# Kernel optimization log

Hardware: AMD Instinct MI355X
Metric: run time of the kernel (lower is better)

The kernel has to match this reference:

```python
import jax, jax.numpy as jnp
import numpy as np

N = 32768      # total nodes (2048 graphs * 16 nodes)
E = 491520     # total edges (2048 graphs * 16*15)
F = 11         # in_node_nf
H = 64         # hidden_nf
G = 2048       # number of graphs
NN = 16        # nodes per graph
R = 1024       # n_reactions
L = 4          # n_layers
EIN = 2 * H + 1        # edge_mlp input: [h[row], h[col], radial]
NIN = H + H + F        # node_mlp input: [h, agg, node_attr=h0]


def setup_inputs() -> dict:
    key = jax.random.key(0)
    ks = jax.random.split(key, 24)
    s = 0.05
    d = {
        "h0": jax.random.normal(ks[0], (N, F), jnp.float32),
        "positions": jax.random.normal(ks[1], (N, 3), jnp.float32),
        "edges": jax.random.randint(ks[2], (2, E), 0, N),
        "node_mask": jnp.ones((N, 1), jnp.float32),
        "edge_mask": jnp.ones((E, 1), jnp.float32),
        "reaction_indexes": jax.random.randint(ks[3], (G,), 0, R),
        "reaction_signs": jax.random.normal(ks[4], (G,), jnp.float32),
        # params
        "emb_w": jax.random.normal(ks[5], (F, H), jnp.float32) * s,
        "emb_b": jnp.zeros((H,), jnp.float32),
        "edge_w1": jax.random.normal(ks[6], (L, EIN, H), jnp.float32) * s,
        "edge_b1": jnp.zeros((L, H), jnp.float32),
        "edge_w2": jax.random.normal(ks[7], (L, H, H), jnp.float32) * s,
        "edge_b2": jnp.zeros((L, H), jnp.float32),
        "node_w1": jax.random.normal(ks[8], (L, NIN, H), jnp.float32) * s,
        "node_b1": jnp.zeros((L, H), jnp.float32),
        "node_w2": jax.random.normal(ks[9], (L, H, H), jnp.float32) * s,
        "node_b2": jnp.zeros((L, H), jnp.float32),
        "dec_w1": jax.random.normal(ks[10], (H, H), jnp.float32) * s,
        "dec_b1": jnp.zeros((H,), jnp.float32),
        "dec_w2": jax.random.normal(ks[11], (H, H), jnp.float32) * s,
        "dec_b2": jnp.zeros((H,), jnp.float32),
        "g_w1": jax.random.normal(ks[12], (H, H), jnp.float32) * s,
        "g_b1": jnp.zeros((H,), jnp.float32),
        "g_w2": jax.random.normal(ks[13], (H, 1), jnp.float32) * s,
        "g_b2": jnp.zeros((1,), jnp.float32),
        "n_nodes": NN,
        "n_reactions": R,
    }
    return d


def reference(h0, positions, edges, node_mask, edge_mask, reaction_indexes,
              reaction_signs, emb_w, emb_b, edge_w1, edge_b1, edge_w2, edge_b2,
              node_w1, node_b1, node_w2, node_b2, dec_w1, dec_b1, dec_w2,
              dec_b2, g_w1, g_b1, g_w2, g_b2, n_nodes, n_reactions):
    silu = jax.nn.silu
    row, col = edges[0], edges[1]
    n = h0.shape[0]

    # radial is constant across layers (coords never updated in this variant)
    coord_diff = positions[row] - positions[col]          # [E, 3]
    radial = jnp.sum(coord_diff ** 2, axis=1, keepdims=True)  # [E, 1]

    h = h0 @ emb_w + emb_b                                # [N, H]
    for i in range(edge_w1.shape[0]):
        # edge model
        e_in = jnp.concatenate([h[row], h[col], radial], axis=1)  # [E, 2H+1]
        e = silu(e_in @ edge_w1[i] + edge_b1[i])
        e = silu(e @ edge_w2[i] + edge_b2[i])             # [E, H]
        e = e * edge_mask
        # scatter-sum aggregation by source node
        agg = jax.ops.segment_sum(e, row, num_segments=n)  # [N, H]
        # node model (node_attr = h0)
        n_in = jnp.concatenate([h, agg, h0], axis=1)      # [N, 2H+F]
        h = silu(n_in @ node_w1[i] + node_b1[i]) @ node_w2[i] + node_b2[i]

    # node decoder
    h = silu(h @ dec_w1 + dec_b1) @ dec_w2 + dec_b2
    h = h * node_mask
    # pool per graph (fixed n_nodes per graph)
    hg = h.reshape(-1, n_nodes, h.shape[-1]).sum(axis=1)  # [G, H]
    # graph decoder
    temp = silu(hg @ g_w1 + g_b1) @ g_w2 + g_b2           # [G, 1]
    # signed per-reaction aggregation
    pred = jnp.zeros((n_reactions,), h.dtype).at[reaction_indexes].add(
        temp[:, 0] * reaction_signs)
    return pred
```

## Files before the change

kernel.cpp:

```cpp
#include <hip/hip_runtime.h>
#include <math.h>

#define N_NODES 32768
#define N_EDGES 491520
#define F_IN    11
#define H       64
#define G_GRAPHS 2048
#define NN_PER_G 16
#define R_REACT 1024
#define L_LAYERS 4
#define EIN     129
#define NIN     139
#define NPBLK   32

typedef __attribute__((ext_vector_type(8))) short short8;
typedef __attribute__((ext_vector_type(4))) float f32x4;

__device__ __forceinline__ float silu_f(float x) {
    return x * __builtin_amdgcn_rcpf(1.0f + __expf(-x));
}
__device__ __forceinline__ void atomAddF(float* p, float v) {
    unsafeAtomicAdd(p, v);
}
__device__ __forceinline__ float bf2f(unsigned short b) {
    union { float f; unsigned u; } v; v.u = ((unsigned)b) << 16;
    return v.f;
}
__device__ __forceinline__ unsigned short f2bf(float x) {
    union { float f; unsigned u; } v; v.f = x;
    unsigned r = v.u + 0x7FFFu + ((v.u >> 16) & 1u);
    return (unsigned short)(r >> 16);
}
__device__ __forceinline__ void splitbf(float x, unsigned short& hi, unsigned short& lo) {
    hi = f2bf(x);
    lo = f2bf(x - bf2f(hi));
}
__device__ __forceinline__ void splitbf_t(float x, unsigned short& hi, unsigned short& lo) {
    union { float f; unsigned u; } v; v.f = x;
    hi = (unsigned short)(v.u >> 16);
    union { float f; unsigned u; } w; w.f = x - bf2f(hi);
    lo = (unsigned short)(w.u >> 16);
}

__global__ __launch_bounds__(256) void k_embed(
        const float* __restrict__ h0, const float* __restrict__ emb_w,
        const float* __restrict__ emb_b, float* __restrict__ h) {
    int tid = blockIdx.x * 256 + threadIdx.x;
    int n = tid >> 6, j = tid & 63;
    float acc = emb_b[j];
#pragma unroll
    for (int k = 0; k < F_IN; ++k)
        acc += h0[n * F_IN + k] * emb_w[k * H + j];
    h[tid] = acc;
}

__global__ __launch_bounds__(256) void k_radial(
        const int* __restrict__ edges, const float* __restrict__ pos,
        float* __restrict__ radial) {
    int e = blockIdx.x * 256 + threadIdx.x;
    int r = edges[e], c = edges[N_EDGES + e];
    float dx = pos[r * 3 + 0] - pos[c * 3 + 0];
    float dy = pos[r * 3 + 1] - pos[c * 3 + 1];
    float dz = pos[r * 3 + 2] - pos[c * 3 + 2];
    radial[e] = dx * dx + dy * dy + dz * dz;
}

__global__ __launch_bounds__(256) void k_hist(
        const int* __restrict__ edges, int* __restrict__ deg) {
    int e = blockIdx.x * 256 + threadIdx.x;
    atomicAdd(&deg[edges[e]], 1);
}

__global__ __launch_bounds__(128) void k_scan_blk(
        const int* __restrict__ deg, int* __restrict__ off,
        int* __restrict__ bsum) {
    __shared__ int sd[128];
    int b = blockIdx.x;
    sd[threadIdx.x] = deg[b * 128 + threadIdx.x];
    __syncthreads();
    if (threadIdx.x == 0) {
        int s = 0;
        for (int i = 0; i < 128; ++i) { int d = sd[i]; sd[i] = s; s += d; }
        bsum[b] = s;
    }
    __syncthreads();
    off[b * 128 + threadIdx.x] = sd[threadIdx.x];
}

__global__ __launch_bounds__(256) void k_scan_top(
        const int* __restrict__ bsum, int* __restrict__ bbase) {
    __shared__ int sb[256];
    sb[threadIdx.x] = bsum[threadIdx.x];
    __syncthreads();
    if (threadIdx.x == 0) {
        int s = 0;
        for (int i = 0; i < 256; ++i) { int d = sb[i]; sb[i] = s; s += d; }
    }
    __syncthreads();
    bbase[threadIdx.x] = sb[threadIdx.x];
}

__global__ __launch_bounds__(256) void k_cursor(
        const int* __restrict__ off, const int* __restrict__ bbase,
        int* __restrict__ nstart, int* __restrict__ cursor) {
    int n = blockIdx.x * 256 + threadIdx.x;
    int ns = off[n] + bbase[n >> 7];
    nstart[n] = ns;
    cursor[n] = ns;
    if (n == 0) nstart[N_NODES] = N_EDGES;
}

__global__ __launch_bounds__(256) void k_fill(
        const int* __restrict__ edges, const float* __restrict__ radial,
        const float* __restrict__ emask, int* __restrict__ cursor,
        int* __restrict__ csrP, float* __restrict__ csrR,
        float* __restrict__ csrM) {
    int e = blockIdx.x * 256 + threadIdx.x;
    int r = edges[e];
    int pos = atomicAdd(&cursor[r], 1);
    csrP[pos] = edges[N_EDGES + e] | ((r & (NPBLK - 1)) << 16);
    csrR[pos] = radial[e];
    csrM[pos] = emask[e];
}

__global__ __launch_bounds__(64, 1) void k_nodeproj_m(
        const float* __restrict__ h, const float* __restrict__ W1,
        const float* __restrict__ b1,
        float* __restrict__ PA, float* __restrict__ PB) {
    const int lane = threadIdx.x;
    const int quad = lane >> 4, m16 = lane & 15;

    short8 Bh[16], Bl[16];
#pragma unroll
    for (int nt = 0; nt < 8; ++nt) {
#pragma unroll
        for (int kf = 0; kf < 2; ++kf) {
            short8 bh, bl;
#pragma unroll
            for (int j = 0; j < 8; ++j) {
                int row = (nt >= 4 ? 64 : 0) + kf * 32 + quad * 8 + j;
                float w = W1[row * H + (nt & 3) * 16 + m16];
                unsigned short hi, lo; splitbf(w, hi, lo);
                bh[j] = (short)hi; bl[j] = (short)lo;
            }
            Bh[nt * 2 + kf] = bh; Bl[nt * 2 + kf] = bl;
        }
    }
    float b1v[4];
#pragma unroll
    for (int nt = 0; nt < 4; ++nt) b1v[nt] = b1[nt * 16 + m16];

    for (int t = 0; t < 2; ++t) {
        const int nb = (blockIdx.x * 2 + t) * 16;
        const float* hp = h + (nb + m16) * H + quad * 8;
        float av[16];
        *(float4*)&av[0]  = *(const float4*)(hp + 0);
        *(float4*)&av[4]  = *(const float4*)(hp + 4);
        *(float4*)&av[8]  = *(const float4*)(hp + 32);
        *(float4*)&av[12] = *(const float4*)(hp + 36);
        short8 Ah0, Ah1, Al0, Al1;
#pragma unroll
        for (int j = 0; j < 8; ++j) {
            unsigned short hi, lo;
            splitbf_t(av[j], hi, lo);     Ah0[j] = (short)hi; Al0[j] = (short)lo;
            splitbf_t(av[8 + j], hi, lo); Ah1[j] = (short)hi; Al1[j] = (short)lo;
        }
        f32x4 acc[8];
#pragma unroll
        for (int nt = 0; nt < 8; ++nt) {
            f32x4 a = {0.0f, 0.0f, 0.0f, 0.0f};
            a = __builtin_amdgcn_mfma_f32_16x16x32_bf16(Ah0, Bh[nt*2+0], a, 0, 0, 0);
            a = __builtin_amdgcn_mfma_f32_16x16x32_bf16(Ah1, Bh[nt*2+1], a, 0, 0, 0);
            a = __builtin_amdgcn_mfma_f32_16x16x32_bf16(Ah0, Bl[nt*2+0], a, 0, 0, 0);
            a = __builtin_amdgcn_mfma_f32_16x16x32_bf16(Ah1, Bl[nt*2+1], a, 0, 0, 0);
            a = __builtin_amdgcn_mfma_f32_16x16x32_bf16(Al0, Bh[nt*2+0], a, 0, 0, 0);
            a = __builtin_amdgcn_mfma_f32_16x16x32_bf16(Al1, Bh[nt*2+1], a, 0, 0, 0);
            acc[nt] = a;
        }
#pragma unroll
        for (int r4 = 0; r4 < 4; ++r4) {
            const int node = nb + quad * 4 + r4;
#pragma unroll
            for (int nt = 0; nt < 4; ++nt)
                PA[node * H + nt * 16 + m16] = acc[nt][r4] + b1v[nt];
#pragma unroll
            for (int nt = 4; nt < 8; ++nt)
                PB[node * H + (nt - 4) * 16 + m16] = acc[nt][r4];
        }
    }
}

__global__ __launch_bounds__(256, 2) void k_edge6(
        const float* __restrict__ PA, const float* __restrict__ PB,
        const int* __restrict__ nstart, const int* __restrict__ csrP,
        const float* __restrict__ csrR, const float* __restrict__ csrM,
        const float* __restrict__ W1,
        const float* __restrict__ W2, const float* __restrict__ b2,
        float* __restrict__ agg) {
    const int tid = threadIdx.x;
    const int lane = tid & 63, wave = tid >> 6;
    const int quad = lane >> 4, m16 = lane & 15;
    const int n0 = blockIdx.x * NPBLK;

    __shared__ float aggld[NPBLK * 68];
    for (int i = tid; i < NPBLK * 68; i += 256) aggld[i] = 0.0f;

    short8 Bh[8], Bl[8];
#pragma unroll
    for (int nt = 0; nt < 4; ++nt) {
#pragma unroll
        for (int kf = 0; kf < 2; ++kf) {
            short8 bh, bl;
#pragma unroll
            for (int j = 0; j < 8; ++j) {
                float w = W2[(kf * 32 + quad * 8 + j) * H + nt * 16 + m16];
                unsigned short hi, lo; splitbf(w, hi, lo);
                bh[j] = (short)hi; bl[j] = (short)lo;
            }
            Bh[nt * 2 + kf] = bh; Bl[nt * 2 + kf] = bl;
        }
    }
    float w1cr[16];
#pragma unroll
    for (int i = 0; i < 16; ++i) {
        int k = (i < 8) ? (quad * 8 + i) : (32 + quad * 8 + (i - 8));
        w1cr[i] = W1[128 * H + k];
    }
    float b2v[4];
#pragma unroll
    for (int nt = 0; nt < 4; ++nt) b2v[nt] = b2[nt * 16 + m16];

    const int start = nstart[n0];
    const int end   = nstart[n0 + NPBLK];
    __syncthreads();

    const int ntiles = (end - start + 15) >> 4;

    float radA = 0.0f, avA[16], bvA[16];
    int rlA = 0;
    int rlqA[4]; float mkqA[4];

    int t = wave;
    bool haveA = t < ntiles;
    if (haveA) {
        const int idx = start + t * 16 + m16;
        const int ss = min(idx, N_EDGES - 1);
        const int pk = csrP[ss];
        radA = csrR[ss];
        const int c = pk & 0xFFFF;
        rlA = pk >> 16;
        const int sb = start + t * 16 + quad * 4;
#pragma unroll
        for (int r4 = 0; r4 < 4; ++r4) {
            int s = sb + r4, s2 = min(s, N_EDGES - 1);
            rlqA[r4] = csrP[s2] >> 16;
            mkqA[r4] = (s < end) ? csrM[s2] : 0.0f;
        }
        const float* par = PA + (n0 + rlA) * H + quad * 8;
        const float* pbr = PB + c * H + quad * 8;
        *(float4*)&avA[0]  = *(const float4*)(par + 0);
        *(float4*)&avA[4]  = *(const float4*)(par + 4);
        *(float4*)&avA[8]  = *(const float4*)(par + 32);
        *(float4*)&avA[12] = *(const float4*)(par + 36);
        *(float4*)&bvA[0]  = *(const float4*)(pbr + 0);
        *(float4*)&bvA[4]  = *(const float4*)(pbr + 4);
        *(float4*)&bvA[8]  = *(const float4*)(pbr + 32);
        *(float4*)&bvA[12] = *(const float4*)(pbr + 36);
    }

    while (haveA) {
        const int tn = t + 4;
        const bool haveB = tn < ntiles;
        float radB = 0.0f, bvB[16];
        int rlB = 0;
        int rlqB[4]; float mkqB[4];
        if (haveB) {
            const int idx = start + tn * 16 + m16;
            const int ss = min(idx, N_EDGES - 1);
            const int pk = csrP[ss];
            radB = csrR[ss];
            const int c = pk & 0xFFFF;
            rlB = pk >> 16;
            const int sb = start + tn * 16 + quad * 4;
#pragma unroll
            for (int r4 = 0; r4 < 4; ++r4) {
                int s = sb + r4, s2 = min(s, N_EDGES - 1);
                rlqB[r4] = csrP[s2] >> 16;
                mkqB[r4] = (s < end) ? csrM[s2] : 0.0f;
            }
            const float* pbr = PB + c * H + quad * 8;
            *(float4*)&bvB[0]  = *(const float4*)(pbr + 0);
            *(float4*)&bvB[4]  = *(const float4*)(pbr + 4);
            *(float4*)&bvB[8]  = *(const float4*)(pbr + 32);
            *(float4*)&bvB[12] = *(const float4*)(pbr + 36);
        }

        short8 Ah0, Ah1, Al0, Al1;
#pragma unroll
        for (int i = 0; i < 8; ++i) {
            unsigned short hi, lo;
            splitbf_t(silu_f(avA[i] + bvA[i] + radA * w1cr[i]), hi, lo);
            Ah0[i] = (short)hi; Al0[i] = (short)lo;
            splitbf_t(silu_f(avA[8+i] + bvA[8+i] + radA * w1cr[8+i]), hi, lo);
            Ah1[i] = (short)hi; Al1[i] = (short)lo;
        }
        f32x4 acc[4];
#pragma unroll
        for (int nt = 0; nt < 4; ++nt) {
            f32x4 a = {0.0f, 0.0f, 0.0f, 0.0f};
            a = __builtin_amdgcn_mfma_f32_16x16x32_bf16(Ah0, Bh[nt*2+0], a, 0, 0, 0);
            a = __builtin_amdgcn_mfma_f32_16x16x32_bf16(Ah1, Bh[nt*2+1], a, 0, 0, 0);
            a = __builtin_amdgcn_mfma_f32_16x16x32_bf16(Ah0, Bl[nt*2+0], a, 0, 0, 0);
            a = __builtin_amdgcn_mfma_f32_16x16x32_bf16(Ah1, Bl[nt*2+1], a, 0, 0, 0);
            a = __builtin_amdgcn_mfma_f32_16x16x32_bf16(Al0, Bh[nt*2+0], a, 0, 0, 0);
            a = __builtin_amdgcn_mfma_f32_16x16x32_bf16(Al1, Bh[nt*2+1], a, 0, 0, 0);
            acc[nt] = a;
        }

#pragma unroll
        for (int nt = 0; nt < 4; ++nt) {
            float oo[4];
#pragma unroll
            for (int r4 = 0; r4 < 4; ++r4)
                oo[r4] = silu_f(acc[nt][r4] + b2v[nt]) * mkqA[r4];
            int cur = rlqA[0]; float s = oo[0];
#pragma unroll
            for (int r4 = 1; r4 < 4; ++r4) {
                if (rlqA[r4] == cur) { s += oo[r4]; }
                else {
                    atomicAdd(&aggld[cur * 68 + nt * 16 + m16], s);
                    cur = rlqA[r4]; s = oo[r4];
                }
            }
            atomicAdd(&aggld[cur * 68 + nt * 16 + m16], s);
        }

        if (haveB) {
            radA = radB; rlA = rlB;
#pragma unroll
            for (int r4 = 0; r4 < 4; ++r4) { rlqA[r4] = rlqB[r4]; mkqA[r4] = mkqB[r4]; }
            const float* par = PA + (n0 + rlA) * H + quad * 8;
            *(float4*)&avA[0]  = *(const float4*)(par + 0);
            *(float4*)&avA[4]  = *(const float4*)(par + 4);
            *(float4*)&avA[8]  = *(const float4*)(par + 32);
            *(float4*)&avA[12] = *(const float4*)(par + 36);
#pragma unroll
            for (int i = 0; i < 16; ++i) bvA[i] = bvB[i];
        }
        t = tn; haveA = haveB;
    }

    __syncthreads();
#pragma unroll
    for (int i = tid; i < NPBLK * 16; i += 256) {
        int n = i >> 4, cb = (i & 15) << 2;
        *(float4*)&agg[(n0 + n) * H + cb] = *(const float4*)&aggld[n * 68 + cb];
    }
}

__global__ __launch_bounds__(64, 1) void k_node_m(
        float* __restrict__ h, const float* __restrict__ agg,
        const float* __restrict__ h0,
        const float* __restrict__ W1, const float* __restrict__ b1,
        const float* __restrict__ W2, const float* __restrict__ b2) {
    const int lane = threadIdx.x;
    const int quad = lane >> 4, m16 = lane & 15;

    short8 B1h[20], B1l[20];
#pragma unroll
    for (int nt = 0; nt < 4; ++nt) {
#pragma unroll
        for (int kf = 0; kf < 5; ++kf) {
            short8 bh, bl;
#pragma unroll
            for (int j = 0; j < 8; ++j) {
                int row = kf * 32 + quad * 8 + j;
                float w = (row < NIN) ? W1[row * H + nt * 16 + m16] : 0.0f;
                unsigned short hi, lo; splitbf(w, hi, lo);
                bh[j] = (short)hi; bl[j] = (short)lo;
            }
            B1h[nt * 5 + kf] = bh; B1l[nt * 5 + kf] = bl;
        }
    }
    short8 B2h[8], B2l[8];
#pragma unroll
    for (int nt = 0; nt < 4; ++nt) {
#pragma unroll
        for (int kf = 0; kf < 2; ++kf) {
            short8 bh, bl;
#pragma unroll
            for (int j = 0; j < 8; ++j) {
                float w = W2[(kf * 32 + quad * 8 + j) * H + nt * 16 + m16];
                unsigned short hi, lo; splitbf(w, hi, lo);
                bh[j] = (short)hi; bl[j] = (short)lo;
            }
            B2h[nt * 2 + kf] = bh; B2l[nt * 2 + kf] = bl;
        }
    }
    float b1v[4], b2v[4];
#pragma unroll
    for (int nt = 0; nt < 4; ++nt) {
        b1v[nt] = b1[nt * 16 + m16];
        b2v[nt] = b2[nt * 16 + m16];
    }

    __shared__ float tld[16 * 68];

    for (int t = 0; t < 2; ++t) {
        const int nb = (blockIdx.x * 2 + t) * 16;
        float a1[5][8];
        const float* hp = h + (nb + m16) * H + quad * 8;
        const float* ap = agg + (nb + m16) * H + quad * 8;
        *(float4*)&a1[0][0] = *(const float4*)(hp + 0);
        *(float4*)&a1[0][4] = *(const float4*)(hp + 4);
        *(float4*)&a1[1][0] = *(const float4*)(hp + 32);
        *(float4*)&a1[1][4] = *(const float4*)(hp + 36);
        *(float4*)&a1[2][0] = *(const float4*)(ap + 0);
        *(float4*)&a1[2][4] = *(const float4*)(ap + 4);
        *(float4*)&a1[3][0] = *(const float4*)(ap + 32);
        *(float4*)&a1[3][4] = *(const float4*)(ap + 36);
        const float* h0p = h0 + (nb + m16) * F_IN;
#pragma unroll
        for (int j = 0; j < 8; ++j) {
            int kk = quad * 8 + j;
            a1[4][j] = (kk < F_IN) ? h0p[kk] : 0.0f;
        }
        short8 A1h[5], A1l[5];
#pragma unroll
        for (int kf = 0; kf < 5; ++kf) {
            short8 ah, al;
#pragma unroll
            for (int j = 0; j < 8; ++j) {
                unsigned short hi, lo; splitbf_t(a1[kf][j], hi, lo);
                ah[j] = (short)hi; al[j] = (short)lo;
            }
            A1h[kf] = ah; A1l[kf] = al;
        }
        f32x4 acc[4];
#pragma unroll
        for (int nt = 0; nt < 4; ++nt) {
            f32x4 a = {0.0f, 0.0f, 0.0f, 0.0f};
#pragma unroll
            for (int kf = 0; kf < 5; ++kf)
                a = __builtin_amdgcn_mfma_f32_16x16x32_bf16(A1h[kf], B1h[nt*5+kf], a, 0, 0, 0);
#pragma unroll
            for (int kf = 0; kf < 5; ++kf)
                a = __builtin_amdgcn_mfma_f32_16x16x32_bf16(A1h[kf], B1l[nt*5+kf], a, 0, 0, 0);
#pragma unroll
            for (int kf = 0; kf < 5; ++kf)
                a = __builtin_amdgcn_mfma_f32_16x16x32_bf16(A1l[kf], B1h[nt*5+kf], a, 0, 0, 0);
            acc[nt] = a;
        }
#pragma unroll
        for (int r4 = 0; r4 < 4; ++r4)
#pragma unroll
            for (int nt = 0; nt < 4; ++nt)
                tld[(quad * 4 + r4) * 68 + nt * 16 + m16] =
                    silu_f(acc[nt][r4] + b1v[nt]);
        __syncthreads();
        float a2[16];
        *(float4*)&a2[0]  = *(const float4*)&tld[m16 * 68 + quad * 8 + 0];
        *(float4*)&a2[4]  = *(const float4*)&tld[m16 * 68 + quad * 8 + 4];
        *(float4*)&a2[8]  = *(const float4*)&tld[m16 * 68 + quad * 8 + 32];
        *(float4*)&a2[12] = *(const float4*)&tld[m16 * 68 + quad * 8 + 36];
        short8 A2h0, A2h1, A2l0, A2l1;
#pragma unroll
        for (int j = 0; j < 8; ++j) {
            unsigned short hi, lo;
            splitbf_t(a2[j], hi, lo);     A2h0[j] = (short)hi; A2l0[j] = (short)lo;
            splitbf_t(a2[8+j], hi, lo);   A2h1[j] = (short)hi; A2l1[j] = (short)lo;
        }
        f32x4 acc2[4];
#pragma unroll
        for (int nt = 0; nt < 4; ++nt) {
            f32x4 a = {0.0f, 0.0f, 0.0f, 0.0f};
            a = __builtin_amdgcn_mfma_f32_16x16x32_bf16(A2h0, B2h[nt*2+0], a, 0, 0, 0);
            a = __builtin_amdgcn_mfma_f32_16x16x32_bf16(A2h1, B2h[nt*2+1], a, 0, 0, 0);
            a = __builtin_amdgcn_mfma_f32_16x16x32_bf16(A2h0, B2l[nt*2+0], a, 0, 0, 0);
            a = __builtin_amdgcn_mfma_f32_16x16x32_bf16(A2h1, B2l[nt*2+1], a, 0, 0, 0);
            a = __builtin_amdgcn_mfma_f32_16x16x32_bf16(A2l0, B2h[nt*2+0], a, 0, 0, 0);
            a = __builtin_amdgcn_mfma_f32_16x16x32_bf16(A2l1, B2h[nt*2+1], a, 0, 0, 0);
            acc2[nt] = a;
        }
#pragma unroll
        for (int r4 = 0; r4 < 4; ++r4) {
            const int node = nb + quad * 4 + r4;
#pragma unroll
            for (int nt = 0; nt < 4; ++nt)
                h[node * H + nt * 16 + m16] = acc2[nt][r4] + b2v[nt];
        }
        __syncthreads();
    }
}

__global__ __launch_bounds__(64, 1) void k_dec_m(
        float* __restrict__ h, const float* __restrict__ nmask,
        const float* __restrict__ W1, const float* __restrict__ b1,
        const float* __restrict__ W2, const float* __restrict__ b2) {
    const int lane = threadIdx.x;
    const int quad = lane >> 4, m16 = lane & 15;

    short8 B1h[8], B1l[8], B2h[8], B2l[8];
#pragma unroll
    for (int nt = 0; nt < 4; ++nt) {
#pragma unroll
        for (int kf = 0; kf < 2; ++kf) {
            short8 bh1, bl1, bh2, bl2;
#pragma unroll
            for (int j = 0; j < 8; ++j) {
                int row = kf * 32 + quad * 8 + j;
                unsigned short hi, lo;
                splitbf(W1[row * H + nt * 16 + m16], hi, lo);
                bh1[j] = (short)hi; bl1[j] = (short)lo;
                splitbf(W2[row * H + nt * 16 + m16], hi, lo);
                bh2[j] = (short)hi; bl2[j] = (short)lo;
            }
            B1h[nt*2+kf] = bh1; B1l[nt*2+kf] = bl1;
            B2h[nt*2+kf] = bh2; B2l[nt*2+kf] = bl2;
        }
    }
    float b1v[4], b2v[4];
#pragma unroll
    for (int nt = 0; nt < 4; ++nt) {
        b1v[nt] = b1[nt * 16 + m16];
        b2v[nt] = b2[nt * 16 + m16];
    }
    __shared__ float tld[16 * 68];

    for (int t = 0; t < 2; ++t) {
        const int nb = (blockIdx.x * 2 + t) * 16;
        const float* hp = h + (nb + m16) * H + quad * 8;
        float av[16];
        *(float4*)&av[0]  = *(const float4*)(hp + 0);
        *(float4*)&av[4]  = *(const float4*)(hp + 4);
        *(float4*)&av[8]  = *(const float4*)(hp + 32);
        *(float4*)&av[12] = *(const float4*)(hp + 36);
        short8 Ah0, Ah1, Al0, Al1;
#pragma unroll
        for (int j = 0; j < 8; ++j) {
            unsigned short hi, lo;
            splitbf_t(av[j], hi, lo);     Ah0[j] = (short)hi; Al0[j] = (short)lo;
            splitbf_t(av[8+j], hi, lo);   Ah1[j] = (short)hi; Al1[j] = (short)lo;
        }
        f32x4 acc[4];
#pragma unroll
        for (int nt = 0; nt < 4; ++nt) {
            f32x4 a = {0.0f, 0.0f, 0.0f, 0.0f};
            a = __builtin_amdgcn_mfma_f32_16x16x32_bf16(Ah0, B1h[nt*2+0], a, 0, 0, 0);
            a = __builtin_amdgcn_mfma_f32_16x16x32_bf16(Ah1, B1h[nt*2+1], a, 0, 0, 0);
            a = __builtin_amdgcn_mfma_f32_16x16x32_bf16(Ah0, B1l[nt*2+0], a, 0, 0, 0);
            a = __builtin_amdgcn_mfma_f32_16x16x32_bf16(Ah1, B1l[nt*2+1], a, 0, 0, 0);
            a = __builtin_amdgcn_mfma_f32_16x16x32_bf16(Al0, B1h[nt*2+0], a, 0, 0, 0);
            a = __builtin_amdgcn_mfma_f32_16x16x32_bf16(Al1, B1h[nt*2+1], a, 0, 0, 0);
            acc[nt] = a;
        }
#pragma unroll
        for (int r4 = 0; r4 < 4; ++r4)
#pragma unroll
            for (int nt = 0; nt < 4; ++nt)
                tld[(quad * 4 + r4) * 68 + nt * 16 + m16] =
                    silu_f(acc[nt][r4] + b1v[nt]);
        __syncthreads();
        float a2[16];
        *(float4*)&a2[0]  = *(const float4*)&tld[m16 * 68 + quad * 8 + 0];
        *(float4*)&a2[4]  = *(const float4*)&tld[m16 * 68 + quad * 8 + 4];
        *(float4*)&a2[8]  = *(const float4*)&tld[m16 * 68 + quad * 8 + 32];
        *(float4*)&a2[12] = *(const float4*)&tld[m16 * 68 + quad * 8 + 36];
        short8 A2h0, A2h1, A2l0, A2l1;
#pragma unroll
        for (int j = 0; j < 8; ++j) {
            unsigned short hi, lo;
            splitbf_t(a2[j], hi, lo);     A2h0[j] = (short)hi; A2l0[j] = (short)lo;
            splitbf_t(a2[8+j], hi, lo);   A2h1[j] = (short)hi; A2l1[j] = (short)lo;
        }
        f32x4 acc2[4];
#pragma unroll
        for (int nt = 0; nt < 4; ++nt) {
            f32x4 a = {0.0f, 0.0f, 0.0f, 0.0f};
            a = __builtin_amdgcn_mfma_f32_16x16x32_bf16(A2h0, B2h[nt*2+0], a, 0, 0, 0);
            a = __builtin_amdgcn_mfma_f32_16x16x32_bf16(A2h1, B2h[nt*2+1], a, 0, 0, 0);
            a = __builtin_amdgcn_mfma_f32_16x16x32_bf16(A2h0, B2l[nt*2+0], a, 0, 0, 0);
            a = __builtin_amdgcn_mfma_f32_16x16x32_bf16(A2h1, B2l[nt*2+1], a, 0, 0, 0);
            a = __builtin_amdgcn_mfma_f32_16x16x32_bf16(A2l0, B2h[nt*2+0], a, 0, 0, 0);
            a = __builtin_amdgcn_mfma_f32_16x16x32_bf16(A2l1, B2h[nt*2+1], a, 0, 0, 0);
            acc2[nt] = a;
        }
#pragma unroll
        for (int r4 = 0; r4 < 4; ++r4) {
            const int node = nb + quad * 4 + r4;
            const float nm = nmask[node];
#pragma unroll
            for (int nt = 0; nt < 4; ++nt)
                h[node * H + nt * 16 + m16] = (acc2[nt][r4] + b2v[nt]) * nm;
        }
        __syncthreads();
    }
}

__global__ __launch_bounds__(64) void k_graph(
        const float* __restrict__ h, const int* __restrict__ rid,
        const float* __restrict__ rsign,
        const float* __restrict__ W1, const float* __restrict__ b1,
        const float* __restrict__ W2, const float* __restrict__ b2,
        float* __restrict__ pred) {
    const int g = blockIdx.x;
    const int lane = threadIdx.x;
    float hgv = 0.0f;
#pragma unroll
    for (int m = 0; m < NN_PER_G; ++m)
        hgv += h[(g * NN_PER_G + m) * H + lane];
    __shared__ __align__(16) float hgs[64];
    hgs[lane] = hgv;
    __syncthreads();
    float acc = b1[lane];
#pragma unroll
    for (int k = 0; k < H; ++k)
        acc += hgs[k] * W1[k * H + lane];
    float part = silu_f(acc) * W2[lane];
#pragma unroll
    for (int off = 32; off > 0; off >>= 1)
        part += __shfl_down(part, off);
    if (lane == 0)
        atomAddF(&pred[rid[g]], (part + b2[0]) * rsign[g]);
}

extern "C" void kernel_launch(void* const* d_in, const int* in_sizes, int n_in,
                              void* d_out, int out_size, void* d_ws, size_t ws_size,
                              hipStream_t stream) {
    const float* h0      = (const float*)d_in[0];
    const float* pos     = (const float*)d_in[1];
    const int*   edges   = (const int*)d_in[2];
    const float* nmask   = (const float*)d_in[3];
    const float* emask   = (const float*)d_in[4];
    const int*   rid     = (const int*)d_in[5];
    const float* rsign   = (const float*)d_in[6];
    const float* emb_w   = (const float*)d_in[7];
    const float* emb_b   = (const float*)d_in[8];
    const float* edge_w1 = (const float*)d_in[9];
    const float* edge_b1 = (const float*)d_in[10];
    const float* edge_w2 = (const float*)d_in[11];
    const float* edge_b2 = (const float*)d_in[12];
    const float* node_w1 = (const float*)d_in[13];
    const float* node_b1 = (const float*)d_in[14];
    const float* node_w2 = (const float*)d_in[15];
    const float* node_b2 = (const float*)d_in[16];
    const float* dec_w1  = (const float*)d_in[17];
    const float* dec_b1  = (const float*)d_in[18];
    const float* dec_w2  = (const float*)d_in[19];
    const float* dec_b2  = (const float*)d_in[20];
    const float* g_w1    = (const float*)d_in[21];
    const float* g_b1    = (const float*)d_in[22];
    const float* g_w2    = (const float*)d_in[23];
    const float* g_b2    = (const float*)d_in[24];

    float* h      = (float*)d_ws;
    float* agg    = h + N_NODES * H;
    float* radial = agg + N_NODES * H;
    float* PA     = radial + N_EDGES;
    float* PB     = PA + N_NODES * H;
    float* csrR   = PB + N_NODES * H;
    float* csrM   = csrR + N_EDGES;
    int*   csrP   = (int*)(csrM + N_EDGES);
    int*   deg    = csrP + N_EDGES;
    int*   off    = deg + N_NODES;
    int*   bsum   = off + N_NODES;
    int*   bbase  = bsum + 256;
    int*   nstart = bbase + 256;
    int*   cursor = nstart + N_NODES + 1;
    float* pred   = (float*)d_out;

    hipMemsetAsync(d_out, 0, R_REACT * sizeof(float), stream);
    hipMemsetAsync(deg, 0, N_NODES * sizeof(int), stream);

    k_embed<<<(N_NODES * H) / 256, 256, 0, stream>>>(h0, emb_w, emb_b, h);
    k_radial<<<N_EDGES / 256, 256, 0, stream>>>(edges, pos, radial);
    k_hist<<<N_EDGES / 256, 256, 0, stream>>>(edges, deg);
    k_scan_blk<<<256, 128, 0, stream>>>(deg, off, bsum);
    k_scan_top<<<1, 256, 0, stream>>>(bsum, bbase);
    k_cursor<<<N_NODES / 256, 256, 0, stream>>>(off, bbase, nstart, cursor);
    k_fill<<<N_EDGES / 256, 256, 0, stream>>>(edges, radial, emask, cursor,
                                              csrP, csrR, csrM);

    for (int i = 0; i < L_LAYERS; ++i) {
        k_nodeproj_m<<<N_NODES / 32, 64, 0, stream>>>(
            h, edge_w1 + i * EIN * H, edge_b1 + i * H, PA, PB);
        k_edge6<<<N_NODES / NPBLK, 256, 0, stream>>>(
            PA, PB, nstart, csrP, csrR, csrM,
            edge_w1 + i * EIN * H,
            edge_w2 + i * H * H, edge_b2 + i * H, agg);
        k_node_m<<<N_NODES / 32, 64, 0, stream>>>(
            h, agg, h0,
            node_w1 + i * NIN * H, node_b1 + i * H,
            node_w2 + i * H * H,   node_b2 + i * H);
    }
    k_dec_m<<<N_NODES / 32, 64, 0, stream>>>(h, nmask, dec_w1, dec_b1,
                                             dec_w2, dec_b2);
    k_graph<<<G_GRAPHS, 64, 0, stream>>>(h, rid, rsign, g_w1, g_b1, g_w2,
                                         g_b2, pred);
}
```

Before: 557.7 us.

## Pre-split weights into bf16 fragment layout once; stage edge W2 lo in LDS

Adds a prep kernel that splits every layer's MLP weights into hi/lo bf16 MFMA fragment layout once per call, stored in workspace. Each per-layer kernel then loads ready-made short8 fragments instead of redoing scattered fp32 loads and splits in every block. The edge kernel also keeps the lo half of W2 in LDS to cut register pressure, and prefetches CSR metadata one extra tile ahead, getting per-row indices and masks via lane shuffles instead of extra global loads. The cost is one more launch, extra workspace, and LDS reads inside the MFMA loop.

```diff
diff --git a/kernel.cpp b/kernel.cpp
--- a/kernel.cpp
+++ b/kernel.cpp
@@ -1,5 +1,6 @@
 #include <hip/hip_runtime.h>
 #include <math.h>
+#include <stdint.h>
 
 #define N_NODES 32768
 #define N_EDGES 491520
@@ -13,6 +14,14 @@
 #define NIN     139
 #define NPBLK   32
 
+#define WPROJ 0
+#define WE2   65536
+#define WN1   98304
+#define WN2   180224
+#define WD1   212992
+#define WD2   221184
+#define WTOT  229376
+
 typedef __attribute__((ext_vector_type(8))) short short8;
 typedef __attribute__((ext_vector_type(4))) float f32x4;
 
@@ -40,6 +49,88 @@
     hi = (unsigned short)(v.u >> 16);
     union { float f; unsigned u; } w; w.f = x - bf2f(hi);
     lo = (unsigned short)(w.u >> 16);
+}
+
+__global__ __launch_bounds__(64) void k_prepw(
+        const float* __restrict__ ew1, const float* __restrict__ ew2,
+        const float* __restrict__ nw1, const float* __restrict__ nw2,
+        const float* __restrict__ dw1, const float* __restrict__ dw2,
+        short* __restrict__ wsW) {
+    const int b = blockIdx.x;
+    const int lane = threadIdx.x;
+    const int quad = lane >> 4, m16 = lane & 15;
+    short8 h8, l8;
+    short* base; int fidx, half;
+
+    if (b < 64) {
+        int l = b >> 4, f = b & 15;
+        int nt = f >> 1, kf = f & 1;
+#pragma unroll
+        for (int j = 0; j < 8; ++j) {
+            int row = (nt >= 4 ? 64 : 0) + kf * 32 + quad * 8 + j;
+            unsigned short hi, lo;
+            splitbf(ew1[l * EIN * H + row * H + (nt & 3) * 16 + m16], hi, lo);
+            h8[j] = (short)hi; l8[j] = (short)lo;
+        }
+        base = wsW + WPROJ + l * 16384; fidx = f; half = 8192;
+    } else if (b < 96) {
+        int bb = b - 64; int l = bb >> 3, f = bb & 7;
+        int nt = f >> 1, kf = f & 1;
+#pragma unroll
+        for (int j = 0; j < 8; ++j) {
+            int row = kf * 32 + quad * 8 + j;
+            unsigned short hi, lo;
+            splitbf(ew2[l * H * H + row * H + nt * 16 + m16], hi, lo);
+            h8[j] = (short)hi; l8[j] = (short)lo;
+        }
+        base = wsW + WE2 + l * 8192; fidx = f; half = 4096;
+    } else if (b < 176) {
+        int bb = b - 96; int l = bb / 20, f = bb % 20;
+        int nt = f / 5, kf = f % 5;
+#pragma unroll
+        for (int j = 0; j < 8; ++j) {
+            int row = kf * 32 + quad * 8 + j;
+            float w = (row < NIN) ? nw1[l * NIN * H + row * H + nt * 16 + m16] : 0.0f;
+            unsigned short hi, lo; splitbf(w, hi, lo);
+            h8[j] = (short)hi; l8[j] = (short)lo;
+        }
+        base = wsW + WN1 + l * 20480; fidx = f; half = 10240;
+    } else if (b < 208) {
+        int bb = b - 176; int l = bb >> 3, f = bb & 7;
+        int nt = f >> 1, kf = f & 1;
+#pragma unroll
+        for (int j = 0; j < 8; ++j) {
+            int row = kf * 32 + quad * 8 + j;
+            unsigned short hi, lo;
+            splitbf(nw2[l * H * H + row * H + nt * 16 + m16], hi, lo);
+            h8[j] = (short)hi; l8[j] = (short)lo;
+        }
+        base = wsW + WN2 + l * 8192; fidx = f; half = 4096;
+    } else if (b < 216) {
+        int f = b - 208;
+        int nt = f >> 1, kf = f & 1;
+#pragma unroll
+        for (int j = 0; j < 8; ++j) {
+            int row = kf * 32 + quad * 8 + j;
+            unsigned short hi, lo;
+            splitbf(dw1[row * H + nt * 16 + m16], hi, lo);
+            h8[j] = (short)hi; l8[j] = (short)lo;
+        }
+        base = wsW + WD1; fidx = f; half = 4096;
+    } else {
+        int f = b - 216;
+        int nt = f >> 1, kf = f & 1;
+#pragma unroll
+        for (int j = 0; j < 8; ++j) {
+            int row = kf * 32 + quad * 8 + j;
+            unsigned short hi, lo;
+            splitbf(dw2[row * H + nt * 16 + m16], hi, lo);
+            h8[j] = (short)hi; l8[j] = (short)lo;
+        }
+        base = wsW + WD2; fidx = f; half = 4096;
+    }
+    *(short8*)(base + (fidx * 64 + lane) * 8) = h8;
+    *(short8*)(base + half + (fidx * 64 + lane) * 8) = l8;
 }
 
 __global__ __launch_bounds__(256) void k_embed(
@@ -124,7 +215,7 @@
 }
 
 __global__ __launch_bounds__(64, 1) void k_nodeproj_m(
-        const float* __restrict__ h, const float* __restrict__ W1,
+        const float* __restrict__ h, const short* __restrict__ wP,
         const float* __restrict__ b1,
         float* __restrict__ PA, float* __restrict__ PB) {
     const int lane = threadIdx.x;
@@ -132,19 +223,9 @@
 
     short8 Bh[16], Bl[16];
 #pragma unroll
-    for (int nt = 0; nt < 8; ++nt) {
-#pragma unroll
-        for (int kf = 0; kf < 2; ++kf) {
-            short8 bh, bl;
-#pragma unroll
-            for (int j = 0; j < 8; ++j) {
-                int row = (nt >= 4 ? 64 : 0) + kf * 32 + quad * 8 + j;
-                float w = W1[row * H + (nt & 3) * 16 + m16];
-                unsigned short hi, lo; splitbf(w, hi, lo);
-                bh[j] = (short)hi; bl[j] = (short)lo;
-            }
-            Bh[nt * 2 + kf] = bh; Bl[nt * 2 + kf] = bl;
-        }
+    for (int f = 0; f < 16; ++f) {
+        Bh[f] = *(const short8*)(wP + (f * 64 + lane) * 8);
+        Bl[f] = *(const short8*)(wP + 8192 + (f * 64 + lane) * 8);
     }
     float b1v[4];
 #pragma unroll
@@ -195,7 +276,7 @@
         const int* __restrict__ nstart, const int* __restrict__ csrP,
         const float* __restrict__ csrR, const float* __restrict__ csrM,
         const float* __restrict__ W1,
-        const float* __restrict__ W2, const float* __restrict__ b2,
+        const short* __restrict__ wE2, const float* __restrict__ b2,
         float* __restrict__ agg) {
     const int tid = threadIdx.x;
     const int lane = tid & 63, wave = tid >> 6;
@@ -203,23 +284,15 @@
     const int n0 = blockIdx.x * NPBLK;
 
     __shared__ float aggld[NPBLK * 68];
+    __shared__ short blds[8 * 64 * 8];
     for (int i = tid; i < NPBLK * 68; i += 256) aggld[i] = 0.0f;
-
-    short8 Bh[8], Bl[8];
-#pragma unroll
-    for (int nt = 0; nt < 4; ++nt) {
-#pragma unroll
-        for (int kf = 0; kf < 2; ++kf) {
-            short8 bh, bl;
-#pragma unroll
-            for (int j = 0; j < 8; ++j) {
-                float w = W2[(kf * 32 + quad * 8 + j) * H + nt * 16 + m16];
-                unsigned short hi, lo; splitbf(w, hi, lo);
-                bh[j] = (short)hi; bl[j] = (short)lo;
-            }
-            Bh[nt * 2 + kf] = bh; Bl[nt * 2 + kf] = bl;
-        }
-    }
+    for (int i = tid; i < 8 * 64; i += 256)
+        *(short8*)(blds + i * 8) = *(const short8*)(wE2 + 4096 + i * 8);
+
+    short8 Bh[8];
+#pragma unroll
+    for (int f = 0; f < 8; ++f)
+        Bh[f] = *(const short8*)(wE2 + (f * 64 + lane) * 8);
     float w1cr[16];
 #pragma unroll
     for (int i = 0; i < 16; ++i) {
@@ -236,27 +309,21 @@
 
     const int ntiles = (end - start + 15) >> 4;
 
-    float radA = 0.0f, avA[16], bvA[16];
-    int rlA = 0;
-    int rlqA[4]; float mkqA[4];
-
-    int t = wave;
-    bool haveA = t < ntiles;
+    int   pkA = 0, pkB = 0;
+    float radA = 0.0f, radB = 0.0f, mkA = 0.0f, mkB = 0.0f;
+    float avA[16], bvA[16];
+
+    int tA = wave;
+    bool haveA = tA < ntiles;
     if (haveA) {
-        const int idx = start + t * 16 + m16;
-        const int ss = min(idx, N_EDGES - 1);
-        const int pk = csrP[ss];
+        const int idx = start + tA * 16 + m16;
+        const int ss  = min(idx, N_EDGES - 1);
+        pkA  = csrP[ss];
         radA = csrR[ss];
-        const int c = pk & 0xFFFF;
-        rlA = pk >> 16;
-        const int sb = start + t * 16 + quad * 4;
-#pragma unroll
-        for (int r4 = 0; r4 < 4; ++r4) {
-            int s = sb + r4, s2 = min(s, N_EDGES - 1);
-            rlqA[r4] = csrP[s2] >> 16;
-            mkqA[r4] = (s < end) ? csrM[s2] : 0.0f;
-        }
-        const float* par = PA + (n0 + rlA) * H + quad * 8;
+        mkA  = (idx < end) ? csrM[ss] : 0.0f;
+        const int c  = pkA & 0xFFFF;
+        const int rl = pkA >> 16;
+        const float* par = PA + (n0 + rl) * H + quad * 8;
         const float* pbr = PB + c * H + quad * 8;
         *(float4*)&avA[0]  = *(const float4*)(par + 0);
         *(float4*)&avA[4]  = *(const float4*)(par + 4);
@@ -267,33 +334,36 @@
         *(float4*)&bvA[8]  = *(const float4*)(pbr + 32);
         *(float4*)&bvA[12] = *(const float4*)(pbr + 36);
     }
+    int tB = tA + 4;
+    bool haveB = tB < ntiles;
+    if (haveB) {
+        const int idx = start + tB * 16 + m16;
+        const int ss  = min(idx, N_EDGES - 1);
+        pkB  = csrP[ss];
+        radB = csrR[ss];
+        mkB  = (idx < end) ? csrM[ss] : 0.0f;
+    }
 
     while (haveA) {
-        const int tn = t + 4;
-        const bool haveB = tn < ntiles;
-        float radB = 0.0f, bvB[16];
-        int rlB = 0;
-        int rlqB[4]; float mkqB[4];
+        float bvB[16];
         if (haveB) {
-            const int idx = start + tn * 16 + m16;
-            const int ss = min(idx, N_EDGES - 1);
-            const int pk = csrP[ss];
-            radB = csrR[ss];
-            const int c = pk & 0xFFFF;
-            rlB = pk >> 16;
-            const int sb = start + tn * 16 + quad * 4;
-#pragma unroll
-            for (int r4 = 0; r4 < 4; ++r4) {
-                int s = sb + r4, s2 = min(s, N_EDGES - 1);
-                rlqB[r4] = csrP[s2] >> 16;
-                mkqB[r4] = (s < end) ? csrM[s2] : 0.0f;
-            }
+            const int c = pkB & 0xFFFF;
             const float* pbr = PB + c * H + quad * 8;
             *(float4*)&bvB[0]  = *(const float4*)(pbr + 0);
             *(float4*)&bvB[4]  = *(const float4*)(pbr + 4);
             *(float4*)&bvB[8]  = *(const float4*)(pbr + 32);
             *(float4*)&bvB[12] = *(const float4*)(pbr + 36);
         }
+        const int tC = tB + 4;
+        const bool haveC = tC < ntiles;
+        int pkC = 0; float radC = 0.0f, mkC = 0.0f;
+        if (haveC) {
+            const int idx = start + tC * 16 + m16;
+            const int ss  = min(idx, N_EDGES - 1);
+            pkC  = csrP[ss];
+            radC = csrR[ss];
+            mkC  = (idx < end) ? csrM[ss] : 0.0f;
+        }
 
         short8 Ah0, Ah1, Al0, Al1;
 #pragma unroll
@@ -310,44 +380,52 @@
             f32x4 a = {0.0f, 0.0f, 0.0f, 0.0f};
             a = __builtin_amdgcn_mfma_f32_16x16x32_bf16(Ah0, Bh[nt*2+0], a, 0, 0, 0);
             a = __builtin_amdgcn_mfma_f32_16x16x32_bf16(Ah1, Bh[nt*2+1], a, 0, 0, 0);
-            a = __builtin_amdgcn_mfma_f32_16x16x32_bf16(Ah0, Bl[nt*2+0], a, 0, 0, 0);
-            a = __builtin_amdgcn_mfma_f32_16x16x32_bf16(Ah1, Bl[nt*2+1], a, 0, 0, 0);
+            short8 bl0 = *(const short8*)(blds + ((nt*2+0) * 64 + lane) * 8);
+            short8 bl1 = *(const short8*)(blds + ((nt*2+1) * 64 + lane) * 8);
+            a = __builtin_amdgcn_mfma_f32_16x16x32_bf16(Ah0, bl0, a, 0, 0, 0);
+            a = __builtin_amdgcn_mfma_f32_16x16x32_bf16(Ah1, bl1, a, 0, 0, 0);
             a = __builtin_amdgcn_mfma_f32_16x16x32_bf16(Al0, Bh[nt*2+0], a, 0, 0, 0);
             a = __builtin_amdgcn_mfma_f32_16x16x32_bf16(Al1, Bh[nt*2+1], a, 0, 0, 0);
             acc[nt] = a;
         }
 
+        int rlq[4]; float mkq[4];
+#pragma unroll
+        for (int r4 = 0; r4 < 4; ++r4) {
+            rlq[r4] = __shfl(pkA, quad * 4 + r4) >> 16;
+            mkq[r4] = __shfl(mkA, quad * 4 + r4);
+        }
 #pragma unroll
         for (int nt = 0; nt < 4; ++nt) {
             float oo[4];
 #pragma unroll
             for (int r4 = 0; r4 < 4; ++r4)
-                oo[r4] = silu_f(acc[nt][r4] + b2v[nt]) * mkqA[r4];
-            int cur = rlqA[0]; float s = oo[0];
+                oo[r4] = silu_f(acc[nt][r4] + b2v[nt]) * mkq[r4];
+            int cur = rlq[0]; float s = oo[0];
 #pragma unroll
             for (int r4 = 1; r4 < 4; ++r4) {
-                if (rlqA[r4] == cur) { s += oo[r4]; }
+                if (rlq[r4] == cur) { s += oo[r4]; }
                 else {
                     atomicAdd(&aggld[cur * 68 + nt * 16 + m16], s);
-                    cur = rlqA[r4]; s = oo[r4];
+                    cur = rlq[r4]; s = oo[r4];
                 }
             }
             atomicAdd(&aggld[cur * 68 + nt * 16 + m16], s);
         }
 
         if (haveB) {
-            radA = radB; rlA = rlB;
-#pragma unroll
-            for (int r4 = 0; r4 < 4; ++r4) { rlqA[r4] = rlqB[r4]; mkqA[r4] = mkqB[r4]; }
-            const float* par = PA + (n0 + rlA) * H + quad * 8;
+            const int rl = pkB >> 16;
+            const float* par = PA + (n0 + rl) * H + quad * 8;
             *(float4*)&avA[0]  = *(const float4*)(par + 0);
             *(float4*)&avA[4]  = *(const float4*)(par + 4);
             *(float4*)&avA[8]  = *(const float4*)(par + 32);
             *(float4*)&avA[12] = *(const float4*)(par + 36);
 #pragma unroll
             for (int i = 0; i < 16; ++i) bvA[i] = bvB[i];
-        }
-        t = tn; haveA = haveB;
+            pkA = pkB; radA = radB; mkA = mkB;
+        }
+        pkB = pkC; radB = radC; mkB = mkC;
+        tB = tC; haveA = haveB; haveB = haveC;
     }
 
     __syncthreads();
@@ -361,41 +439,22 @@
 __global__ __launch_bounds__(64, 1) void k_node_m(
         float* __restrict__ h, const float* __restrict__ agg,
         const float* __restrict__ h0,
-        const float* __restrict__ W1, const float* __restrict__ b1,
-        const float* __restrict__ W2, const float* __restrict__ b2) {
+        const short* __restrict__ wN1, const float* __restrict__ b1,
+        const short* __restrict__ wN2, const float* __restrict__ b2) {
     const int lane = threadIdx.x;
     const int quad = lane >> 4, m16 = lane & 15;
 
     short8 B1h[20], B1l[20];
 #pragma unroll
-    for (int nt = 0; nt < 4; ++nt) {
-#pragma unroll
-        for (int kf = 0; kf < 5; ++kf) {
-            short8 bh, bl;
-#pragma unroll
-            for (int j = 0; j < 8; ++j) {
-                int row = kf * 32 + quad * 8 + j;
-                float w = (row < NIN) ? W1[row * H + nt * 16 + m16] : 0.0f;
-                unsigned short hi, lo; splitbf(w, hi, lo);
-                bh[j] = (short)hi; bl[j] = (short)lo;
-            }
-            B1h[nt * 5 + kf] = bh; B1l[nt * 5 + kf] = bl;
-        }
+    for (int f = 0; f < 20; ++f) {
+        B1h[f] = *(const short8*)(wN1 + (f * 64 + lane) * 8);
+        B1l[f] = *(const short8*)(wN1 + 10240 + (f * 64 + lane) * 8);
     }
     short8 B2h[8], B2l[8];
 #pragma unroll
-    for (int nt = 0; nt < 4; ++nt) {
-#pragma unroll
-        for (int kf = 0; kf < 2; ++kf) {
-            short8 bh, bl;
-#pragma unroll
-            for (int j = 0; j < 8; ++j) {
-                float w = W2[(kf * 32 + quad * 8 + j) * H + nt * 16 + m16];
-                unsigned short hi, lo; splitbf(w, hi, lo);
-                bh[j] = (short)hi; bl[j] = (short)lo;
-            }
-            B2h[nt * 2 + kf] = bh; B2l[nt * 2 + kf] = bl;
-        }
+    for (int f = 0; f < 8; ++f) {
+        B2h[f] = *(const short8*)(wN2 + (f * 64 + lane) * 8);
+        B2l[f] = *(const short8*)(wN2 + 4096 + (f * 64 + lane) * 8);
     }
     float b1v[4], b2v[4];
 #pragma unroll
@@ -495,29 +554,18 @@
 
 __global__ __launch_bounds__(64, 1) void k_dec_m(
         float* __restrict__ h, const float* __restrict__ nmask,
-        const float* __restrict__ W1, const float* __restrict__ b1,
-        const float* __restrict__ W2, const float* __restrict__ b2) {
+        const short* __restrict__ wD1, const float* __restrict__ b1,
+        const short* __restrict__ wD2, const float* __restrict__ b2) {
     const int lane = threadIdx.x;
     const int quad = lane >> 4, m16 = lane & 15;
 
     short8 B1h[8], B1l[8], B2h[8], B2l[8];
 #pragma unroll
-    for (int nt = 0; nt < 4; ++nt) {
-#pragma unroll
-        for (int kf = 0; kf < 2; ++kf) {
-            short8 bh1, bl1, bh2, bl2;
-#pragma unroll
-            for (int j = 0; j < 8; ++j) {
-                int row = kf * 32 + quad * 8 + j;
-                unsigned short hi, lo;
-                splitbf(W1[row * H + nt * 16 + m16], hi, lo);
-                bh1[j] = (short)hi; bl1[j] = (short)lo;
-                splitbf(W2[row * H + nt * 16 + m16], hi, lo);
-                bh2[j] = (short)hi; bl2[j] = (short)lo;
-            }
-            B1h[nt*2+kf] = bh1; B1l[nt*2+kf] = bl1;
-            B2h[nt*2+kf] = bh2; B2l[nt*2+kf] = bl2;
-        }
+    for (int f = 0; f < 8; ++f) {
+        B1h[f] = *(const short8*)(wD1 + (f * 64 + lane) * 8);
+        B1l[f] = *(const short8*)(wD1 + 4096 + (f * 64 + lane) * 8);
+        B2h[f] = *(const short8*)(wD2 + (f * 64 + lane) * 8);
+        B2l[f] = *(const short8*)(wD2 + 4096 + (f * 64 + lane) * 8);
     }
     float b1v[4], b2v[4];
 #pragma unroll
@@ -667,11 +715,14 @@
     int*   bbase  = bsum + 256;
     int*   nstart = bbase + 256;
     int*   cursor = nstart + N_NODES + 1;
+    short* wsW    = (short*)((((uintptr_t)(cursor + N_NODES)) + 255) & ~(uintptr_t)255);
     float* pred   = (float*)d_out;
 
     hipMemsetAsync(d_out, 0, R_REACT * sizeof(float), stream);
     hipMemsetAsync(deg, 0, N_NODES * sizeof(int), stream);
 
+    k_prepw<<<224, 64, 0, stream>>>(edge_w1, edge_w2, node_w1, node_w2,
+                                    dec_w1, dec_w2, wsW);
     k_embed<<<(N_NODES * H) / 256, 256, 0, stream>>>(h0, emb_w, emb_b, h);
     k_radial<<<N_EDGES / 256, 256, 0, stream>>>(edges, pos, radial);
     k_hist<<<N_EDGES / 256, 256, 0, stream>>>(edges, deg);
@@ -683,18 +734,18 @@
 
     for (int i = 0; i < L_LAYERS; ++i) {
         k_nodeproj_m<<<N_NODES / 32, 64, 0, stream>>>(
-            h, edge_w1 + i * EIN * H, edge_b1 + i * H, PA, PB);
+            h, wsW + WPROJ + i * 16384, edge_b1 + i * H, PA, PB);
         k_edge6<<<N_NODES / NPBLK, 256, 0, stream>>>(
             PA, PB, nstart, csrP, csrR, csrM,
             edge_w1 + i * EIN * H,
-            edge_w2 + i * H * H, edge_b2 + i * H, agg);
+            wsW + WE2 + i * 8192, edge_b2 + i * H, agg);
         k_node_m<<<N_NODES / 32, 64, 0, stream>>>(
             h, agg, h0,
-            node_w1 + i * NIN * H, node_b1 + i * H,
-            node_w2 + i * H * H,   node_b2 + i * H);
-    }
-    k_dec_m<<<N_NODES / 32, 64, 0, stream>>>(h, nmask, dec_w1, dec_b1,
-                                             dec_w2, dec_b2);
+            wsW + WN1 + i * 20480, node_b1 + i * H,
+            wsW + WN2 + i * 8192,  node_b2 + i * H);
+    }
+    k_dec_m<<<N_NODES / 32, 64, 0, stream>>>(h, nmask, wsW + WD1, dec_b1,
+                                             wsW + WD2, dec_b2);
     k_graph<<<G_GRAPHS, 64, 0, stream>>>(h, rid, rsign, g_w1, g_b1, g_w2,
                                          g_b2, pred);
 }
```

After: 563.6 us. No clear change (+1.1%).
